# Optimization experiments

Measured on AMD Instinct MI355X. Metric: run time of the kernel, lower is better.

## Reference

```python
import jax, jax.numpy as jnp
import numpy as np


def setup_inputs() -> dict:
    key = jax.random.key(0)
    k1, k2, k3, k4 = jax.random.split(key, 4)
    B, N_LEAVES, D_IN, L, C = 64, 512, 512, 5, 4
    n_nodes = 2 * N_LEAVES - 1  # heap layout: node i has children 2i+1, 2i+2
    h = jax.random.normal(k1, (B, n_nodes, D_IN), dtype=jnp.float32)
    W = jax.random.normal(k2, (D_IN, L * C), dtype=jnp.float32) * (1.0 / np.sqrt(D_IN))
    b = jax.random.normal(k3, (L * C,), dtype=jnp.float32) * 0.02
    trans = jax.random.normal(k4, (L, L, L, C, C, C), dtype=jnp.float32) * 0.1
    return {"h": h, "W": W, "b": b, "trans": trans}


def reference(h, W, b, trans):
    """Batched inside algorithm of BinaryTreeLatentVariable.forward.

    h: [B, n_nodes, D] node hidden states (complete binary tree, heap order).
    Returns root inside score [B, L, C].
    """
    B, n_nodes, _ = h.shape
    L = trans.shape[0]
    C = trans.shape[3]
    n_leaves = (n_nodes + 1) // 2
    depth = int(np.log2(n_leaves))

    # Emission: state_weight_layer applied to every node at once.
    sw = (h @ W + b).reshape(B, n_nodes, L, C)  # [B, N, L, C]

    # Leaves: in_weight = state_weight. Internal slots overwritten bottom-up.
    in_w = sw
    for d in range(depth - 1, -1, -1):  # level-synchronous, bottom-up
        start, end = 2 ** d - 1, 2 ** (d + 1) - 1  # internal nodes of this level
        l = in_w[:, 2 * start + 1:2 * end:2]        # [B, m, L, C] left children
        r = in_w[:, 2 * start + 2:2 * end + 1:2]    # [B, m, L, C] right children
        p = sw[:, start:end]                        # [B, m, L, C] parent emission
        # score[b,m, pL,lL,rL, pc,lc,rc]
        score = (p[:, :, :, None, None, :, None, None]
                 + l[:, :, None, :, None, None, :, None]
                 + r[:, :, None, None, :, None, None, :]
                 + trans)
        new = jax.nn.logsumexp(score, axis=(3, 4, 6, 7))  # marginalize children
        in_w = in_w.at[:, start:end].set(new)
    return in_w[:, 0]  # root inside score [B, L, C]
```

## Files before the change

### kernel.cpp

```cpp
#include <hip/hip_runtime.h>
#include <hip/hip_bf16.h>
#include <math.h>

#define NB      64
#define NNODES  1023
#define LC      20
#define DIN     512
#define NROWS   (NB * NNODES)
#define ET_PAD  404

#define BM      64
#define BK      64
#define NKC     (DIN / BK)
#define SCP     21

typedef unsigned short u16;
typedef short bf16x8 __attribute__((ext_vector_type(8)));
typedef float f32x4  __attribute__((ext_vector_type(4)));

__device__ __forceinline__ u16 f2bf(float f) {
    unsigned x = __float_as_uint(f);
    return (u16)((x + 0x7FFFu + ((x >> 16) & 1u)) >> 16);
}

__global__ __launch_bounds__(256) void prep_kernel(
    const float* __restrict__ trans, const float* __restrict__ W,
    float* __restrict__ ET, u16* __restrict__ Bfrag)
{
    int t = blockIdx.x * 256 + threadIdx.x;
    if (t < 8000) {
        int q   = t % 20;
        int rem = t / 20;
        int j   = rem % 20;
        int i   = rem / 20;
        int ll = i >> 2, cl = i & 3;
        int lr = j >> 2, cr = j & 3;
        int lp = q >> 2, cp = q & 3;
        int src = ((((lp * 5 + ll) * 5 + lr) * 4 + cp) * 4 + cl) * 4 + cr;
        ET[q * ET_PAD + i * 20 + j] = expf(trans[src]);
    }
    if (t < 1280) {
        int col, kb;
        if (t < 1024) {
            int lane = t & 63, ks = t >> 6;
            col = lane & 15;
            kb  = ks * 32 + ((lane >> 4) & 3) * 8;
        } else {
            int idx = t - 1024;
            int ks = idx >> 4, g = (idx >> 2) & 3, c = idx & 3;
            col = 16 + c;
            kb  = ks * 32 + g * 8;
        }
        unsigned e[8];
        #pragma unroll
        for (int j = 0; j < 8; ++j)
            e[j] = (unsigned)f2bf(W[(kb + j) * LC + col]);
        uint4 v;
        v.x = e[0] | (e[1] << 16); v.y = e[2] | (e[3] << 16);
        v.z = e[4] | (e[5] << 16); v.w = e[6] | (e[7] << 16);
        ((uint4*)Bfrag)[t] = v;
    }
}

__global__ __launch_bounds__(256, 4) void gemm_kernel(
    const float* __restrict__ h, const u16* __restrict__ Bfrag,
    const float* __restrict__ bias, float* __restrict__ buf)
{
    __shared__ u16  AsU[2][BM][64];
    __shared__ uint4 Bs[1280];
    const int t    = threadIdx.x;
    const int lane = t & 63;
    const int wv   = t >> 6;
    const size_t row0 = (size_t)blockIdx.x * BM;

    #pragma unroll
    for (int i = 0; i < 5; ++i)
        Bs[t + 256 * i] = ((const uint4*)Bfrag)[t + 256 * i];

    const int srow = t >> 4;
    const int sk4  = t & 15;
    const int woff = (((sk4 >> 1) ^ (srow & 7)) << 3) + ((sk4 & 1) << 2);
    const float* hp0 = h + (row0 + srow) * DIN + sk4 * 4;
    const float* hp1 = hp0 + 16 * DIN;
    const float* hp2 = hp0 + 32 * DIN;
    const float* hp3 = hp0 + 48 * DIN;

    f32x4 acc00 = {0.f,0.f,0.f,0.f}, acc01 = {0.f,0.f,0.f,0.f};
    float4 R0[4], R1[4], R2[4];
    const uint4 z4 = make_uint4(0u, 0u, 0u, 0u);

#define ISSUE(RB, CC) {                                                       \
    RB[0] = *(const float4*)(hp0 + (CC) * BK);                                \
    RB[1] = *(const float4*)(hp1 + (CC) * BK);                                \
    RB[2] = *(const float4*)(hp2 + (CC) * BK);                                \
    RB[3] = *(const float4*)(hp3 + (CC) * BK); }

#define CVTWRITE(RB, P) { u16* _b = &AsU[P][0][0] + woff; _Pragma("unroll")   \
    for (int i = 0; i < 4; ++i) {                                             \
        uint2 pk;                                                             \
        pk.x = (unsigned)f2bf(RB[i].x) | ((unsigned)f2bf(RB[i].y) << 16);     \
        pk.y = (unsigned)f2bf(RB[i].z) | ((unsigned)f2bf(RB[i].w) << 16);     \
        *(uint2*)(_b + (srow + 16 * i) * 64) = pk; } }

#define BCOMP(P, C) {                                                         \
    const u16* _ab = &AsU[P][0][0] + (wv * 16 + (lane & 15)) * 64;            \
    int _r0 = (((lane >> 4)    ) ^ (lane & 7)) << 3;                          \
    int _r1 = (((lane >> 4) + 4) ^ (lane & 7)) << 3;                          \
    bf16x8 _a0 = *(const bf16x8*)(_ab + _r0);                                 \
    bf16x8 _a1 = *(const bf16x8*)(_ab + _r1);                                 \
    uint4 _b00 = Bs[(2 * (C)    ) * 64 + lane];                               \
    uint4 _b02 = Bs[(2 * (C) + 1) * 64 + lane];                               \
    uint4 _b10 = Bs[1024 + (2 * (C)    ) * 16 + ((lane >> 4) << 2) + (lane & 3)]; \
    uint4 _b12 = Bs[1024 + (2 * (C) + 1) * 16 + ((lane >> 4) << 2) + (lane & 3)]; \
    if ((lane & 15) >= 4) { _b10 = z4; _b12 = z4; }                           \
    acc00 = __builtin_amdgcn_mfma_f32_16x16x32_bf16(                          \
        _a0, __builtin_bit_cast(bf16x8, _b00), acc00, 0, 0, 0);               \
    acc01 = __builtin_amdgcn_mfma_f32_16x16x32_bf16(                          \
        _a0, __builtin_bit_cast(bf16x8, _b10), acc01, 0, 0, 0);               \
    acc00 = __builtin_amdgcn_mfma_f32_16x16x32_bf16(                          \
        _a1, __builtin_bit_cast(bf16x8, _b02), acc00, 0, 0, 0);               \
    acc01 = __builtin_amdgcn_mfma_f32_16x16x32_bf16(                          \
        _a1, __builtin_bit_cast(bf16x8, _b12), acc01, 0, 0, 0); }

#define BAR() { asm volatile("s_waitcnt lgkmcnt(0)" ::: "memory");            \
                __builtin_amdgcn_s_barrier(); }

    ISSUE(R0, 0); ISSUE(R1, 1); ISSUE(R2, 2);
    CVTWRITE(R0, 0);
    BAR();
    BCOMP(0, 0); ISSUE(R0, 3); CVTWRITE(R1, 1); BAR();
    BCOMP(1, 1); ISSUE(R1, 4); CVTWRITE(R2, 0); BAR();
    BCOMP(0, 2); ISSUE(R2, 5); CVTWRITE(R0, 1); BAR();
    BCOMP(1, 3); ISSUE(R0, 6); CVTWRITE(R1, 0); BAR();
    BCOMP(0, 4); ISSUE(R1, 7); CVTWRITE(R2, 1); BAR();
    BCOMP(1, 5);               CVTWRITE(R0, 0); BAR();
    BCOMP(0, 6);               CVTWRITE(R1, 1); BAR();
    BCOMP(1, 7);
#undef ISSUE
#undef CVTWRITE
#undef BCOMP
#undef BAR

    float* sc = (float*)&AsU[0][0][0];
    #pragma unroll
    for (int nf = 0; nf < 2; ++nf) {
        f32x4 a = nf ? acc01 : acc00;
        int col = nf * 16 + (lane & 15);
        if (col < LC) {
            float bv = bias[col];
            #pragma unroll
            for (int p = 0; p < 4; ++p) {
                int rl = wv * 16 + (lane >> 4) * 4 + p;
                sc[rl * SCP + col] = a[p] + bv;
            }
        }
    }
    __syncthreads();
    {
        float4* dst = (float4*)(buf + row0 * LC);
        int f0 = t * 4;
        float4 o;
        o.x = sc[((f0 + 0) / 20) * SCP + (f0 + 0) % 20];
        o.y = sc[((f0 + 1) / 20) * SCP + (f0 + 1) % 20];
        o.z = sc[((f0 + 2) / 20) * SCP + (f0 + 2) % 20];
        o.w = sc[((f0 + 3) / 20) * SCP + (f0 + 3) % 20];
        dst[t] = o;
        if (t < 64) {
            int p = 256 + t, g0 = p * 4;
            float4 o2;
            o2.x = sc[((g0 + 0) / 20) * SCP + (g0 + 0) % 20];
            o2.y = sc[((g0 + 1) / 20) * SCP + (g0 + 1) % 20];
            o2.z = sc[((g0 + 2) / 20) * SCP + (g0 + 2) % 20];
            o2.w = sc[((g0 + 3) / 20) * SCP + (g0 + 3) % 20];
            dst[p] = o2;
        }
    }
}

__device__ __forceinline__ void level_body(
    float* __restrict__ buf, const float* __restrict__ et,
    float* __restrict__ out, int bi, int node, int q)
{
    size_t pbase = ((size_t)bi * NNODES + node) * LC;
    size_t lbase = ((size_t)bi * NNODES + 2 * node + 1) * LC;

    float l[LC], r[LC];
    const float4* l4 = (const float4*)(buf + lbase);
    const float4* r4 = (const float4*)(buf + lbase + LC);
    #pragma unroll
    for (int v = 0; v < 5; ++v) {
        float4 lv = l4[v], rv = r4[v];
        l[4*v+0] = lv.x; l[4*v+1] = lv.y; l[4*v+2] = lv.z; l[4*v+3] = lv.w;
        r[4*v+0] = rv.x; r[4*v+1] = rv.y; r[4*v+2] = rv.z; r[4*v+3] = rv.w;
    }
    float maxl = l[0], maxr = r[0];
    #pragma unroll
    for (int i = 1; i < LC; ++i) {
        maxl = fmaxf(maxl, l[i]);
        maxr = fmaxf(maxr, r[i]);
    }
    float el[LC], er[LC];
    #pragma unroll
    for (int i = 0; i < LC; ++i) {
        el[i] = __expf(l[i] - maxl);
        er[i] = __expf(r[i] - maxr);
    }

    const float4* etq = (const float4*)(et + q * ET_PAD);
    float s = 0.f;
    #pragma unroll
    for (int i = 0; i < LC; ++i) {
        float4 e0 = etq[i*5+0], e1 = etq[i*5+1], e2 = etq[i*5+2],
               e3 = etq[i*5+3], e4 = etq[i*5+4];
        float d0 = 0.f, d1 = 0.f;
        d0 = fmaf(e0.x, er[0],  d0); d1 = fmaf(e0.y, er[1],  d1);
        d0 = fmaf(e0.z, er[2],  d0); d1 = fmaf(e0.w, er[3],  d1);
        d0 = fmaf(e1.x, er[4],  d0); d1 = fmaf(e1.y, er[5],  d1);
        d0 = fmaf(e1.z, er[6],  d0); d1 = fmaf(e1.w, er[7],  d1);
        d0 = fmaf(e2.x, er[8],  d0); d1 = fmaf(e2.y, er[9],  d1);
        d0 = fmaf(e2.z, er[10], d0); d1 = fmaf(e2.w, er[11], d1);
        d0 = fmaf(e3.x, er[12], d0); d1 = fmaf(e3.y, er[13], d1);
        d0 = fmaf(e3.z, er[14], d0); d1 = fmaf(e3.w, er[15], d1);
        d0 = fmaf(e4.x, er[16], d0); d1 = fmaf(e4.y, er[17], d1);
        d0 = fmaf(e4.z, er[18], d0); d1 = fmaf(e4.w, er[19], d1);
        s = fmaf(el[i], d0 + d1, s);
    }

    float val = buf[pbase + q] + maxl + maxr + __logf(s);
    buf[pbase + q] = val;
    if (out) out[(size_t)bi * LC + q] = val;
}

__global__ __launch_bounds__(256) void level_kernel(
    float* __restrict__ buf, const float* __restrict__ ETg,
    int start, int count)
{
    __shared__ float et[LC * ET_PAD];
    for (int idx = threadIdx.x; idx < LC * ET_PAD / 4; idx += 256)
        ((float4*)et)[idx] = ((const float4*)ETg)[idx];
    __syncthreads();

    int t  = blockIdx.x * 256 + threadIdx.x;
    int pj = t / LC;
    int q  = t - pj * LC;
    if (pj >= NB * count) return;
    int bi   = pj / count;
    int node = start + (pj - bi * count);
    level_body(buf, et, nullptr, bi, node, q);
}

__global__ __launch_bounds__(640) void tail_kernel(
    float* __restrict__ buf, const float* __restrict__ ETg,
    float* __restrict__ out)
{
    __shared__ float et[LC * ET_PAD];
    for (int idx = threadIdx.x; idx < LC * ET_PAD / 4; idx += 640)
        ((float4*)et)[idx] = ((const float4*)ETg)[idx];
    __syncthreads();

    const int bi = blockIdx.x;
    for (int d = 6; d >= 0; --d) {
        int count = 1 << d;
        int start = count - 1;
        int total = count * LC;
        for (int base = 0; base < total; base += 640) {
            int idx = base + (int)threadIdx.x;
            if (idx < total) {
                int node = start + idx / LC;
                int q    = idx % LC;
                level_body(buf, et, (d == 0) ? out : nullptr, bi, node, q);
            }
        }
        __syncthreads();
    }
}

extern "C" void kernel_launch(void* const* d_in, const int* in_sizes, int n_in,
                              void* d_out, int out_size, void* d_ws, size_t ws_size,
                              hipStream_t stream)
{
    const float* h     = (const float*)d_in[0];
    const float* W     = (const float*)d_in[1];
    const float* bias  = (const float*)d_in[2];
    const float* trans = (const float*)d_in[3];

    char* ws = (char*)d_ws;
    float* ET    = (float*)(ws);
    u16*   Bfrag = (u16*)(ws + 32768);
    float* buf   = (float*)(ws + 32768 + 24576);

    prep_kernel<<<32, 256, 0, stream>>>(trans, W, ET, Bfrag);

    gemm_kernel<<<NROWS / BM, 256, 0, stream>>>(h, Bfrag, bias, buf);

    for (int d = 8; d >= 7; --d) {
        int count = 1 << d;
        int start = count - 1;
        int T = NB * count * LC;
        level_kernel<<<(T + 255) / 256, 256, 0, stream>>>(buf, ET, start, count);
    }
    tail_kernel<<<NB, 640, 0, stream>>>(buf, ET, (float*)d_out);
}
```

Before: 71.72 us.

## Load GEMM A fragments directly from global into registers, bypassing LDS staging

The GEMM kernel no longer stages h tiles through a double-buffered, swizzled LDS buffer with per-chunk barriers. Each lane now loads its own MFMA A-fragment (8 floats) straight from global memory, converts it to bf16 in registers, and keeps a two-chunk register prefetch. The K loop drops from eight 64-wide chunks to sixteen 32-wide steps, and launch bounds are raised to 5 blocks per CU because LDS use shrinks. This removes LDS write/read traffic and the barriers inside the loop. In exchange, each lane's global reads cover only 32 bytes per row segment, which is less coalesced than the old row-wide loads.

```diff
diff --git a/kernel.cpp b/kernel.cpp
--- a/kernel.cpp
+++ b/kernel.cpp
@@ -10,8 +10,6 @@
 #define ET_PAD  404
 
 #define BM      64
-#define BK      64
-#define NKC     (DIN / BK)
 #define SCP     21
 
 typedef unsigned short u16;
@@ -42,14 +40,14 @@
     if (t < 1280) {
         int col, kb;
         if (t < 1024) {
-            int lane = t & 63, ks = t >> 6;
+            int lane = t & 63, cg = t >> 6;
             col = lane & 15;
-            kb  = ks * 32 + ((lane >> 4) & 3) * 8;
+            kb  = cg * 32 + ((lane >> 4) & 3) * 8;
         } else {
             int idx = t - 1024;
-            int ks = idx >> 4, g = (idx >> 2) & 3, c = idx & 3;
+            int cg = idx >> 4, g = (idx >> 2) & 3, c = idx & 3;
             col = 16 + c;
-            kb  = ks * 32 + g * 8;
+            kb  = cg * 32 + g * 8;
         }
         unsigned e[8];
         #pragma unroll
@@ -62,116 +60,93 @@
     }
 }
 
-__global__ __launch_bounds__(256, 4) void gemm_kernel(
+__global__ __launch_bounds__(256, 5) void gemm_kernel(
     const float* __restrict__ h, const u16* __restrict__ Bfrag,
     const float* __restrict__ bias, float* __restrict__ buf)
 {
-    __shared__ u16  AsU[2][BM][64];
     __shared__ uint4 Bs[1280];
+    __shared__ float scT[BM * SCP];
     const int t    = threadIdx.x;
     const int lane = t & 63;
     const int wv   = t >> 6;
     const size_t row0 = (size_t)blockIdx.x * BM;
 
-    #pragma unroll
-    for (int i = 0; i < 5; ++i)
-        Bs[t + 256 * i] = ((const uint4*)Bfrag)[t + 256 * i];
-
-    const int srow = t >> 4;
-    const int sk4  = t & 15;
-    const int woff = (((sk4 >> 1) ^ (srow & 7)) << 3) + ((sk4 & 1) << 2);
-    const float* hp0 = h + (row0 + srow) * DIN + sk4 * 4;
-    const float* hp1 = hp0 + 16 * DIN;
-    const float* hp2 = hp0 + 32 * DIN;
-    const float* hp3 = hp0 + 48 * DIN;
-
-    f32x4 acc00 = {0.f,0.f,0.f,0.f}, acc01 = {0.f,0.f,0.f,0.f};
-    float4 R0[4], R1[4], R2[4];
+    Bs[t] = ((const uint4*)Bfrag)[t];
+    Bs[t + 256] = ((const uint4*)Bfrag)[t + 256];
+    Bs[t + 512] = ((const uint4*)Bfrag)[t + 512];
+    Bs[t + 768] = ((const uint4*)Bfrag)[t + 768];
+    Bs[t + 1024] = ((const uint4*)Bfrag)[t + 1024];
+
+    const float4* ap4 = (const float4*)
+        (h + (row0 + wv * 16 + (lane & 15)) * DIN + ((lane >> 4) << 3));
+
+    f32x4 acc0 = {0.f,0.f,0.f,0.f}, acc1 = {0.f,0.f,0.f,0.f};
     const uint4 z4 = make_uint4(0u, 0u, 0u, 0u);
 
-#define ISSUE(RB, CC) {                                                       \
-    RB[0] = *(const float4*)(hp0 + (CC) * BK);                                \
-    RB[1] = *(const float4*)(hp1 + (CC) * BK);                                \
-    RB[2] = *(const float4*)(hp2 + (CC) * BK);                                \
-    RB[3] = *(const float4*)(hp3 + (CC) * BK); }
-
-#define CVTWRITE(RB, P) { u16* _b = &AsU[P][0][0] + woff; _Pragma("unroll")   \
-    for (int i = 0; i < 4; ++i) {                                             \
-        uint2 pk;                                                             \
-        pk.x = (unsigned)f2bf(RB[i].x) | ((unsigned)f2bf(RB[i].y) << 16);     \
-        pk.y = (unsigned)f2bf(RB[i].z) | ((unsigned)f2bf(RB[i].w) << 16);     \
-        *(uint2*)(_b + (srow + 16 * i) * 64) = pk; } }
-
-#define BCOMP(P, C) {                                                         \
-    const u16* _ab = &AsU[P][0][0] + (wv * 16 + (lane & 15)) * 64;            \
-    int _r0 = (((lane >> 4)    ) ^ (lane & 7)) << 3;                          \
-    int _r1 = (((lane >> 4) + 4) ^ (lane & 7)) << 3;                          \
-    bf16x8 _a0 = *(const bf16x8*)(_ab + _r0);                                 \
-    bf16x8 _a1 = *(const bf16x8*)(_ab + _r1);                                 \
-    uint4 _b00 = Bs[(2 * (C)    ) * 64 + lane];                               \
-    uint4 _b02 = Bs[(2 * (C) + 1) * 64 + lane];                               \
-    uint4 _b10 = Bs[1024 + (2 * (C)    ) * 16 + ((lane >> 4) << 2) + (lane & 3)]; \
-    uint4 _b12 = Bs[1024 + (2 * (C) + 1) * 16 + ((lane >> 4) << 2) + (lane & 3)]; \
-    if ((lane & 15) >= 4) { _b10 = z4; _b12 = z4; }                           \
-    acc00 = __builtin_amdgcn_mfma_f32_16x16x32_bf16(                          \
-        _a0, __builtin_bit_cast(bf16x8, _b00), acc00, 0, 0, 0);               \
-    acc01 = __builtin_amdgcn_mfma_f32_16x16x32_bf16(                          \
-        _a0, __builtin_bit_cast(bf16x8, _b10), acc01, 0, 0, 0);               \
-    acc00 = __builtin_amdgcn_mfma_f32_16x16x32_bf16(                          \
-        _a1, __builtin_bit_cast(bf16x8, _b02), acc00, 0, 0, 0);               \
-    acc01 = __builtin_amdgcn_mfma_f32_16x16x32_bf16(                          \
-        _a1, __builtin_bit_cast(bf16x8, _b12), acc01, 0, 0, 0); }
-
-#define BAR() { asm volatile("s_waitcnt lgkmcnt(0)" ::: "memory");            \
-                __builtin_amdgcn_s_barrier(); }
-
-    ISSUE(R0, 0); ISSUE(R1, 1); ISSUE(R2, 2);
-    CVTWRITE(R0, 0);
-    BAR();
-    BCOMP(0, 0); ISSUE(R0, 3); CVTWRITE(R1, 1); BAR();
-    BCOMP(1, 1); ISSUE(R1, 4); CVTWRITE(R2, 0); BAR();
-    BCOMP(0, 2); ISSUE(R2, 5); CVTWRITE(R0, 1); BAR();
-    BCOMP(1, 3); ISSUE(R0, 6); CVTWRITE(R1, 0); BAR();
-    BCOMP(0, 4); ISSUE(R1, 7); CVTWRITE(R2, 1); BAR();
-    BCOMP(1, 5);               CVTWRITE(R0, 0); BAR();
-    BCOMP(0, 6);               CVTWRITE(R1, 1); BAR();
-    BCOMP(1, 7);
-#undef ISSUE
-#undef CVTWRITE
-#undef BCOMP
-#undef BAR
-
-    float* sc = (float*)&AsU[0][0][0];
-    #pragma unroll
-    for (int nf = 0; nf < 2; ++nf) {
-        f32x4 a = nf ? acc01 : acc00;
-        int col = nf * 16 + (lane & 15);
-        if (col < LC) {
-            float bv = bias[col];
+    float4 pa0 = ap4[0], pb0 = ap4[1];
+    float4 pa1 = ap4[8], pb1 = ap4[9];
+
+    asm volatile("s_waitcnt lgkmcnt(0)" ::: "memory");
+    __builtin_amdgcn_s_barrier();
+
+    #pragma unroll
+    for (int c = 0; c < 16; ++c) {
+        float4 x0, x1;
+        if (c & 1) { x0 = pa1; x1 = pb1; }
+        else       { x0 = pa0; x1 = pb0; }
+        if (c + 2 < 16) {
+            if (c & 1) { pa1 = ap4[(c + 2) * 8]; pb1 = ap4[(c + 2) * 8 + 1]; }
+            else       { pa0 = ap4[(c + 2) * 8]; pb0 = ap4[(c + 2) * 8 + 1]; }
+        }
+        unsigned e0 = (unsigned)f2bf(x0.x) | ((unsigned)f2bf(x0.y) << 16);
+        unsigned e1 = (unsigned)f2bf(x0.z) | ((unsigned)f2bf(x0.w) << 16);
+        unsigned e2 = (unsigned)f2bf(x1.x) | ((unsigned)f2bf(x1.y) << 16);
+        unsigned e3 = (unsigned)f2bf(x1.z) | ((unsigned)f2bf(x1.w) << 16);
+        uint4 au = make_uint4(e0, e1, e2, e3);
+        bf16x8 af = __builtin_bit_cast(bf16x8, au);
+
+        uint4 b0 = Bs[c * 64 + lane];
+        uint4 b1 = Bs[1024 + c * 16 + ((lane >> 4) << 2) + (lane & 3)];
+        if ((lane & 15) >= 4) b1 = z4;
+
+        acc0 = __builtin_amdgcn_mfma_f32_16x16x32_bf16(
+            af, __builtin_bit_cast(bf16x8, b0), acc0, 0, 0, 0);
+        acc1 = __builtin_amdgcn_mfma_f32_16x16x32_bf16(
+            af, __builtin_bit_cast(bf16x8, b1), acc1, 0, 0, 0);
+    }
+
+    {
+        int col0 = lane & 15;
+        int r0   = wv * 16 + ((lane >> 4) << 2);
+        float bv0 = bias[col0];
+        #pragma unroll
+        for (int p = 0; p < 4; ++p)
+            scT[(r0 + p) * SCP + col0] = acc0[p] + bv0;
+        if (col0 < 4) {
+            float bv1 = bias[16 + col0];
             #pragma unroll
-            for (int p = 0; p < 4; ++p) {
-                int rl = wv * 16 + (lane >> 4) * 4 + p;
-                sc[rl * SCP + col] = a[p] + bv;
-            }
-        }
-    }
-    __syncthreads();
+            for (int p = 0; p < 4; ++p)
+                scT[(r0 + p) * SCP + 16 + col0] = acc1[p] + bv1;
+        }
+    }
+    asm volatile("s_waitcnt lgkmcnt(0)" ::: "memory");
+    __builtin_amdgcn_s_barrier();
     {
         float4* dst = (float4*)(buf + row0 * LC);
         int f0 = t * 4;
         float4 o;
-        o.x = sc[((f0 + 0) / 20) * SCP + (f0 + 0) % 20];
-        o.y = sc[((f0 + 1) / 20) * SCP + (f0 + 1) % 20];
-        o.z = sc[((f0 + 2) / 20) * SCP + (f0 + 2) % 20];
-        o.w = sc[((f0 + 3) / 20) * SCP + (f0 + 3) % 20];
+        o.x = scT[((f0 + 0) / 20) * SCP + (f0 + 0) % 20];
+        o.y = scT[((f0 + 1) / 20) * SCP + (f0 + 1) % 20];
+        o.z = scT[((f0 + 2) / 20) * SCP + (f0 + 2) % 20];
+        o.w = scT[((f0 + 3) / 20) * SCP + (f0 + 3) % 20];
         dst[t] = o;
         if (t < 64) {
             int p = 256 + t, g0 = p * 4;
             float4 o2;
-            o2.x = sc[((g0 + 0) / 20) * SCP + (g0 + 0) % 20];
-            o2.y = sc[((g0 + 1) / 20) * SCP + (g0 + 1) % 20];
-            o2.z = sc[((g0 + 2) / 20) * SCP + (g0 + 2) % 20];
-            o2.w = sc[((g0 + 3) / 20) * SCP + (g0 + 3) % 20];
+            o2.x = scT[((g0 + 0) / 20) * SCP + (g0 + 0) % 20];
+            o2.y = scT[((g0 + 1) / 20) * SCP + (g0 + 1) % 20];
+            o2.z = scT[((g0 + 2) / 20) * SCP + (g0 + 2) % 20];
+            o2.w = scT[((g0 + 3) / 20) * SCP + (g0 + 3) % 20];
             dst[p] = o2;
         }
     }
```

New measurement: 74.11 us. +3.3%, slower.
